# Kernel optimization log

Measured on AMD Instinct MI355X. Metric: run time of the kernel, lower is better.

The kernel has to match this reference:

```python
import jax, jax.numpy as jnp
import numpy as np

N_LAYERS, B, H, D = 24, 16, 32, 64
E = H * D            # 2048
TS_H = 32            # token_shift_hidden_dim
N_BRANCH = 5         # key, receptance, decay, value, bonus
GN_EPS = 1e-3        # keras GroupNormalization default epsilon


def setup_inputs() -> dict:
    key = jax.random.key(0)
    ks = jax.random.split(key, 20)
    s = 0.02
    return {
        "inputs": jax.random.normal(ks[0], (B, E), jnp.float32),
        "state": jax.random.normal(ks[1], (N_LAYERS, 1, B, E), jnp.float32),
        "state_matrix": jax.random.normal(ks[2], (N_LAYERS, B, H, D, D), jnp.float32),
        # stacked branch params, order: key, receptance, decay, value, bonus
        "mus": jax.random.normal(ks[3], (N_BRANCH, E), jnp.float32) * s,
        "lambdas": jax.random.normal(ks[4], (N_BRANCH, E), jnp.float32) * s,
        "Aw": jax.random.normal(ks[5], (N_BRANCH, E, TS_H), jnp.float32) * s,
        "Ab": jnp.zeros((N_BRANCH, TS_H), jnp.float32),
        "Bw": jax.random.normal(ks[6], (N_BRANCH, TS_H, E), jnp.float32) * s,
        "Bb": jnp.zeros((N_BRANCH, E), jnp.float32),
        "MW": jax.random.normal(ks[7], (N_BRANCH, H, D, D), jnp.float32) * s,
        "Mb": jnp.zeros((N_BRANCH, H, D), jnp.float32),
        "gate_mu": jax.random.normal(ks[8], (E,), jnp.float32) * s,
        "gate_W": jax.random.normal(ks[9], (E, E), jnp.float32) * s,
        "gate_b": jnp.zeros((E,), jnp.float32),
        "gn_gamma": jnp.ones((E,), jnp.float32),
        "gn_beta": jnp.zeros((E,), jnp.float32),
        "out_W": jax.random.normal(ks[10], (E, E), jnp.float32) * s,
        "out_b": jnp.zeros((E,), jnp.float32),
        "layer_id": 12,
    }


def reference(inputs, state, state_matrix, mus, lambdas, Aw, Ab, Bw, Bb, MW, Mb,
              gate_mu, gate_W, gate_b, gn_gamma, gn_beta, out_W, out_b, layer_id):
    x = inputs                       # [B, E]
    last_x = state[layer_id, 0]      # [B, E]
    diff = x - last_x

    # ddlerp token shift for all 5 branches at once:
    # lora(x + diff*mu) = lambda + tanh(. @ A) @ B ; out = x + lora * diff
    lora_in = x[None] + diff[None] * mus[:, None]                      # [5, B, E]
    hdn = jnp.tanh(jnp.einsum('sbe,seh->sbh', lora_in, Aw) + Ab[:, None])
    lora = jnp.einsum('sbh,she->sbe', hdn, Bw) + Bb[:, None] + lambdas[:, None]
    ts = (lora * diff[None] + x[None]).reshape(N_BRANCH, B, H, D)      # [5, B, H, D]

    # per-head dense for each branch
    proj = jnp.einsum('sbhd,shde->sbhe', ts, MW) + Mb[:, None]         # [5, B, H, D]
    k, r, w_raw, v, u = proj[0], proj[1], proj[2], proj[3], proj[4]

    g = (x * gate_mu + last_x * (1.0 - gate_mu)) @ gate_W + gate_b     # [B, E]

    kv = k[..., :, None] * v[..., None, :]                             # [B, H, D, D]
    w = jnp.exp(-jnp.exp(w_raw))[..., None]                            # [B, H, D, 1]
    S = state_matrix[layer_id]                                         # [B, H, D, D]
    wkv = kv * u[..., None] + S
    new_S = w * S + kv
    rwkv = jnp.einsum('bhij,bhj->bhi', wkv, r)                         # [B, H, D]

    # group norm: num_heads groups over channel axis
    mean = rwkv.mean(-1, keepdims=True)
    var = rwkv.var(-1, keepdims=True)
    normed = ((rwkv - mean) / jnp.sqrt(var + GN_EPS)).reshape(B, E)
    normed = normed * gn_gamma + gn_beta

    time_mixed = (normed * jax.nn.silu(g)) @ out_W + out_b             # [B, E]

    new_state = state.at[layer_id, 0].set(inputs)
    new_state_matrix = state_matrix.at[layer_id].set(new_S)
    return time_mixed, new_state, new_state_matrix
```

## Files before the change

kernel.cpp:

```cpp
#include <hip/hip_runtime.h>
#include <math.h>

#define NL 24
#define BB 16
#define HH 32
#define DD 64
#define EE 2048
#define TSH 32
#define NB 5
#define BE (BB*EE)
#define STATE_N (NL*BB*EE)
#define GN_EPS 1e-3f

#define NCH 11776
#define C1 2400
#define C2 2200
#define C3 2400
#define C4 2200
#define C5 1776
#define C6 800

__device__ __forceinline__ void sm_chunk(int c, int lid, const float4* __restrict__ sm4,
                                         float4* __restrict__ out4, int tid) {
    int l = c >> 9, rr = c & 511;
    int ls = l + (l >= lid);
    const float4* src = sm4 + (long)(ls * 512 + rr) * 1024;
    float4*       dst = out4 + (long)(ls * 512 + rr) * 1024;
    #pragma unroll
    for (int p = 0; p < 4; ++p) dst[p * 256 + tid] = src[p * 256 + tid];
}

__global__ __launch_bounds__(256) void k1_hdn(
    const float* __restrict__ inputs, const float* __restrict__ state,
    const float* __restrict__ mus, const float* __restrict__ Aw,
    const float* __restrict__ Ab, float* __restrict__ hdn,
    const float4* __restrict__ state4, const float4* __restrict__ inputs4,
    float4* __restrict__ out_state4, float* __restrict__ out_tm,
    float* __restrict__ g, const float* __restrict__ out_b,
    const float* __restrict__ gate_b,
    const float4* __restrict__ sm4, float4* __restrict__ out_sm4,
    const int* __restrict__ lid_p)
{
    int blk = blockIdx.x, tid = threadIdx.x;
    int lid = *lid_p;
    if (blk >= 1104) {
        sm_chunk(blk - 1104, lid, sm4, out_sm4, tid);
        return;
    }
    if (blk >= 848) {
        int idx = (blk - 848) * 256 + tid;
        if (idx < BE) out_tm[idx] = out_b[idx & (EE - 1)];
        else g[idx - BE] = gate_b[(idx - BE) & (EE - 1)];
        return;
    }
    if (blk >= 80) {
        int i = (blk - 80) * 256 + tid;
        int lo = lid * (BE / 4);
        float4 v = (i >= lo && i < lo + BE / 4) ? inputs4[i - lo] : state4[i];
        out_state4[i] = v;
        return;
    }
    int s = blk / BB, b = blk % BB;
    __shared__ float li[EE];
    const float* x  = inputs + b * EE;
    const float* lx = state + lid * BE + b * EE;
    const float* mu = mus + s * EE;
    for (int e = tid; e < EE; e += 256) {
        float xv = x[e];
        li[e] = xv + (xv - lx[e]) * mu[e];
    }
    __syncthreads();
    int h = tid & 31, part = tid >> 5;
    const float* A = Aw + s * EE * TSH;
    float acc = 0.f;
    int e0 = part * 256;
    #pragma unroll 8
    for (int e = e0; e < e0 + 256; ++e) acc += li[e] * A[e * TSH + h];
    __shared__ float red[32][9];
    red[h][part] = acc;
    __syncthreads();
    if (tid < 32) {
        float sum = Ab[s * TSH + tid];
        #pragma unroll
        for (int p = 0; p < 8; ++p) sum += red[tid][p];
        hdn[(s * BB + b) * TSH + tid] = tanhf(sum);
    }
}

__global__ __launch_bounds__(256) void k2_ts(
    const float* __restrict__ inputs, const float* __restrict__ state,
    const float* __restrict__ lambdas, const float* __restrict__ Bw,
    const float* __restrict__ Bb, const float* __restrict__ hdn,
    const float* __restrict__ gate_mu, float* __restrict__ ts,
    float* __restrict__ gx,
    const float4* __restrict__ sm4, float4* __restrict__ out_sm4,
    const int* __restrict__ lid_p)
{
    int blk = blockIdx.x, tid = threadIdx.x;
    int lid = *lid_p;
    if (blk >= 640) {
        sm_chunk(C1 + blk - 640, lid, sm4, out_sm4, tid);
        return;
    }
    int idx = blk * 256 + tid;
    int s = idx / BE, r = idx % BE;
    int b = r / EE, e = r % EE;
    const float* hp = hdn + (s * BB + b) * TSH;
    const float* Bp = Bw + s * TSH * EE + e;
    float acc = Bb[s * EE + e] + lambdas[s * EE + e];
    #pragma unroll
    for (int h = 0; h < TSH; ++h) acc += hp[h] * Bp[h * EE];
    float xv = inputs[r];
    float lxv = state[lid * BE + r];
    ts[idx] = acc * (xv - lxv) + xv;
    if (s == 0) {
        float gm = gate_mu[e];
        gx[r] = xv * gm + lxv * (1.f - gm);
    }
}

__global__ __launch_bounds__(256) void k3_proj(
    const float* __restrict__ ts, const float* __restrict__ MW,
    const float* __restrict__ Mb, float* __restrict__ proj,
    const float4* __restrict__ sm4, float4* __restrict__ out_sm4,
    const int* __restrict__ lid_p)
{
    int bi = blockIdx.x, tid = threadIdx.x;
    if (bi >= 640) {
        int lid = *lid_p;
        sm_chunk(C1 + C2 + bi - 640, lid, sm4, out_sm4, tid);
        return;
    }
    int s = bi / (BB * 8);
    int r = bi % (BB * 8);
    int b = r / 8, hg = r % 8;
    int q = tid >> 6, e = tid & 63;
    int h = hg * 4 + q;
    __shared__ float tl[4][DD];
    tl[q][e] = ts[((s * BB + b) * HH + h) * DD + e];
    __syncthreads();
    const float* M = MW + (s * HH + h) * DD * DD;
    float acc = Mb[(s * HH + h) * DD + e];
    #pragma unroll 8
    for (int d = 0; d < DD; ++d) acc += tl[q][d] * M[d * DD + e];
    proj[((s * BB + b) * HH + h) * DD + e] = acc;
}

template <bool SILU>
__device__ __forceinline__ void mm_block(
    int t, const float* __restrict__ Arows, const float* __restrict__ Grows,
    const float* __restrict__ W, float* __restrict__ out, int tid)
{
    int et = t & 7, kc = t >> 3;
    int e = et * 256 + tid;
    int k0 = kc * 64;
    __shared__ float As[BB][64];
    for (int i = tid; i < BB * 64; i += 256) {
        int b = i >> 6, kk = i & 63;
        float av = Arows[b * EE + k0 + kk];
        if constexpr (SILU) {
            float gv = Grows[b * EE + k0 + kk];
            av *= gv / (1.f + expf(-gv));
        }
        As[b][kk] = av;
    }
    __syncthreads();
    float acc[BB];
    #pragma unroll
    for (int b = 0; b < BB; ++b) acc[b] = 0.f;
    #pragma unroll 8
    for (int kk = 0; kk < 64; ++kk) {
        float wv = W[(k0 + kk) * EE + e];
        #pragma unroll
        for (int b = 0; b < BB; ++b) acc[b] += As[b][kk] * wv;
    }
    #pragma unroll
    for (int b = 0; b < BB; ++b) atomicAdd(&out[b * EE + e], acc[b]);
}

__global__ __launch_bounds__(256) void k4_gate(
    const float* __restrict__ gx, const float* __restrict__ gate_W,
    float* __restrict__ g,
    const float4* __restrict__ sm4, float4* __restrict__ out_sm4,
    const int* __restrict__ lid_p)
{
    int blk = blockIdx.x, tid = threadIdx.x;
    if (blk < 256) { mm_block<false>(blk, gx, nullptr, gate_W, g, tid); return; }
    int lid = *lid_p;
    sm_chunk(C1 + C2 + C3 + blk - 256, lid, sm4, out_sm4, tid);
}

__global__ __launch_bounds__(256) void k5_rwkv(
    const float4* __restrict__ sm4, float4* __restrict__ out_sm4,
    const float* __restrict__ proj,
    const float* __restrict__ gn_gamma, const float* __restrict__ gn_beta,
    float* __restrict__ a_out, const int* __restrict__ lid_p)
{
    int blk = blockIdx.x, tid = threadIdx.x;
    int lid = *lid_p;
    if (blk >= 512) {
        sm_chunk(C1 + C2 + C3 + C4 + blk - 512, lid, sm4, out_sm4, tid);
        return;
    }
    int b = blk / HH, h = blk % HH;
    long base4 = (long)(lid * BB * HH + blk) * (DD * DD / 4);
    int j = tid & 63, q = tid >> 6;
    const float* P = proj + (b * HH + h) * DD + j;
    float kv   = P[0 * BE];
    float rv   = P[1 * BE];
    float wraw = P[2 * BE];
    float vv   = P[3 * BE];
    float uv   = P[4 * BE];
    float wv = expf(-expf(wraw));
    float vr = vv * rv;
    #pragma unroll
    for (int o = 32; o; o >>= 1) vr += __shfl_xor(vr, o);
    __shared__ float rw[DD];
    const float* S = (const float*)(sm4 + base4);
    float* NS = (float*)(out_sm4 + base4);
    for (int ii = 0; ii < 16; ii += 4) {
        int i0 = q * 16 + ii;
        float sv[4], kk[4], ww[4], uu[4], pp[4];
        #pragma unroll
        for (int t = 0; t < 4; ++t) {
            sv[t] = S[(i0 + t) * DD + j];
            kk[t] = __shfl(kv, i0 + t);
            ww[t] = __shfl(wv, i0 + t);
            uu[t] = __shfl(uv, i0 + t);
        }
        #pragma unroll
        for (int t = 0; t < 4; ++t) {
            NS[(i0 + t) * DD + j] = ww[t] * sv[t] + kk[t] * vv;
            pp[t] = sv[t] * rv;
        }
        #pragma unroll
        for (int o = 32; o; o >>= 1) {
            #pragma unroll
            for (int t = 0; t < 4; ++t) pp[t] += __shfl_xor(pp[t], o);
        }
        if (j == 0) {
            #pragma unroll
            for (int t = 0; t < 4; ++t) rw[i0 + t] = kk[t] * uu[t] * vr + pp[t];
        }
    }
    __syncthreads();
    if (tid < DD) {
        float xv = rw[tid];
        float m = xv;
        #pragma unroll
        for (int o = 32; o; o >>= 1) m += __shfl_xor(m, o);
        m *= (1.f / 64.f);
        float d = xv - m;
        float var = d * d;
        #pragma unroll
        for (int o = 32; o; o >>= 1) var += __shfl_xor(var, o);
        var *= (1.f / 64.f);
        float normed = d * rsqrtf(var + GN_EPS);
        int e = h * DD + tid;
        a_out[b * EE + e] = normed * gn_gamma[e] + gn_beta[e];
    }
}

__global__ __launch_bounds__(256) void k6_out(
    const float* __restrict__ a, const float* __restrict__ g,
    const float* __restrict__ out_W, float* __restrict__ out_tm,
    const float4* __restrict__ sm4, float4* __restrict__ out_sm4,
    const int* __restrict__ lid_p)
{
    int blk = blockIdx.x, tid = threadIdx.x;
    if (blk < 256) { mm_block<true>(blk, a, g, out_W, out_tm, tid); return; }
    int lid = *lid_p;
    sm_chunk(C1 + C2 + C3 + C4 + C5 + blk - 256, lid, sm4, out_sm4, tid);
}

extern "C" void kernel_launch(void* const* d_in, const int* in_sizes, int n_in,
                              void* d_out, int out_size, void* d_ws, size_t ws_size,
                              hipStream_t stream) {
    const float* inputs   = (const float*)d_in[0];
    const float* state    = (const float*)d_in[1];
    const float* sm       = (const float*)d_in[2];
    const float* mus      = (const float*)d_in[3];
    const float* lambdas  = (const float*)d_in[4];
    const float* Aw       = (const float*)d_in[5];
    const float* Ab       = (const float*)d_in[6];
    const float* Bw       = (const float*)d_in[7];
    const float* Bb       = (const float*)d_in[8];
    const float* MW       = (const float*)d_in[9];
    const float* Mb       = (const float*)d_in[10];
    const float* gate_mu  = (const float*)d_in[11];
    const float* gate_W   = (const float*)d_in[12];
    const float* gate_b   = (const float*)d_in[13];
    const float* gn_gamma = (const float*)d_in[14];
    const float* gn_beta  = (const float*)d_in[15];
    const float* out_W    = (const float*)d_in[16];
    const float* out_b    = (const float*)d_in[17];
    const int*   lid      = (const int*)d_in[18];

    float* out_tm    = (float*)d_out;
    float* out_state = out_tm + BE;
    float* out_sm    = out_state + STATE_N;

    float* ws   = (float*)d_ws;
    float* ts   = ws;
    float* proj = ts + NB * BE;
    float* hdn  = proj + NB * BE;
    float* gx   = hdn + NB * BB * TSH;
    float* g    = gx + BE;
    float* a    = g + BE;

    k1_hdn<<<1104 + C1, 256, 0, stream>>>(inputs, state, mus, Aw, Ab, hdn,
        (const float4*)state, (const float4*)inputs, (float4*)out_state,
        out_tm, g, out_b, gate_b, (const float4*)sm, (float4*)out_sm, lid);
    k2_ts<<<640 + C2, 256, 0, stream>>>(inputs, state, lambdas, Bw, Bb, hdn,
        gate_mu, ts, gx, (const float4*)sm, (float4*)out_sm, lid);
    k3_proj<<<640 + C3, 256, 0, stream>>>(ts, MW, Mb, proj,
        (const float4*)sm, (float4*)out_sm, lid);
    k4_gate<<<256 + C4, 256, 0, stream>>>(gx, gate_W, g,
        (const float4*)sm, (float4*)out_sm, lid);
    k5_rwkv<<<512 + C5, 256, 0, stream>>>((const float4*)sm, (float4*)out_sm,
        proj, gn_gamma, gn_beta, a, lid);
    k6_out<<<256 + C6, 256, 0, stream>>>(a, g, out_W, out_tm,
        (const float4*)sm, (float4*)out_sm, lid);
}
```

Baseline: 442.5 us.

## Merge gate matmul into projection kernel, move gx to k1, use nontemporal copies

Moves the gate input mix (gx) computation into the first kernel and merges the gate matmul blocks into the per-head projection kernel, cutting the launch count from six to five. The state-matrix copy chunk split across kernels is rebalanced to fit the new schedule. The bulk state and state-matrix copies now use nontemporal loads and stores so they bypass the cache and leave room for the compute data. The risk is an uneven chunk split that lengthens some kernels, and nontemporal hints may not help on this hardware.

```diff
diff --git a/kernel.cpp b/kernel.cpp
--- a/kernel.cpp
+++ b/kernel.cpp
@@ -13,51 +13,69 @@
 #define GN_EPS 1e-3f
 
 #define NCH 11776
-#define C1 2400
-#define C2 2200
-#define C3 2400
-#define C4 2200
-#define C5 1776
-#define C6 800
-
-__device__ __forceinline__ void sm_chunk(int c, int lid, const float4* __restrict__ sm4,
-                                         float4* __restrict__ out4, int tid) {
+#define C1 2700
+#define C2 2500
+#define C3 2100
+#define C4 2400
+#define C5 2076
+
+typedef float nt4 __attribute__((ext_vector_type(4)));
+
+__device__ __forceinline__ void sm_chunk(int c, int lid, const nt4* __restrict__ sm4,
+                                         nt4* __restrict__ out4, int tid) {
     int l = c >> 9, rr = c & 511;
     int ls = l + (l >= lid);
-    const float4* src = sm4 + (long)(ls * 512 + rr) * 1024;
-    float4*       dst = out4 + (long)(ls * 512 + rr) * 1024;
-    #pragma unroll
-    for (int p = 0; p < 4; ++p) dst[p * 256 + tid] = src[p * 256 + tid];
+    const nt4* src = sm4 + (long)(ls * 512 + rr) * 1024;
+    nt4*       dst = out4 + (long)(ls * 512 + rr) * 1024;
+    #pragma unroll
+    for (int p = 0; p < 4; ++p) {
+        nt4 v = __builtin_nontemporal_load(&src[p * 256 + tid]);
+        __builtin_nontemporal_store(v, &dst[p * 256 + tid]);
+    }
 }
 
 __global__ __launch_bounds__(256) void k1_hdn(
     const float* __restrict__ inputs, const float* __restrict__ state,
     const float* __restrict__ mus, const float* __restrict__ Aw,
     const float* __restrict__ Ab, float* __restrict__ hdn,
-    const float4* __restrict__ state4, const float4* __restrict__ inputs4,
-    float4* __restrict__ out_state4, float* __restrict__ out_tm,
+    const nt4* __restrict__ state4, const float4* __restrict__ inputs4,
+    nt4* __restrict__ out_state4, float* __restrict__ out_tm,
     float* __restrict__ g, const float* __restrict__ out_b,
-    const float* __restrict__ gate_b,
-    const float4* __restrict__ sm4, float4* __restrict__ out_sm4,
+    const float* __restrict__ gate_b, const float* __restrict__ gate_mu,
+    float* __restrict__ gx,
+    const nt4* __restrict__ sm4, nt4* __restrict__ out_sm4,
     const int* __restrict__ lid_p)
 {
     int blk = blockIdx.x, tid = threadIdx.x;
     int lid = *lid_p;
-    if (blk >= 1104) {
-        sm_chunk(blk - 1104, lid, sm4, out_sm4, tid);
+    if (blk >= 1232) {
+        sm_chunk(blk - 1232, lid, sm4, out_sm4, tid);
         return;
     }
     if (blk >= 848) {
         int idx = (blk - 848) * 256 + tid;
         if (idx < BE) out_tm[idx] = out_b[idx & (EE - 1)];
-        else g[idx - BE] = gate_b[(idx - BE) & (EE - 1)];
+        else if (idx < 2 * BE) g[idx - BE] = gate_b[(idx - BE) & (EE - 1)];
+        else {
+            int r = idx - 2 * BE;
+            float xv = inputs[r];
+            float lxv = state[lid * BE + r];
+            float gm = gate_mu[r & (EE - 1)];
+            gx[r] = xv * gm + lxv * (1.f - gm);
+        }
         return;
     }
     if (blk >= 80) {
         int i = (blk - 80) * 256 + tid;
         int lo = lid * (BE / 4);
-        float4 v = (i >= lo && i < lo + BE / 4) ? inputs4[i - lo] : state4[i];
-        out_state4[i] = v;
+        if (i >= lo && i < lo + BE / 4) {
+            float4 v = inputs4[i - lo];
+            nt4 w = { v.x, v.y, v.z, v.w };
+            __builtin_nontemporal_store(w, &out_state4[i]);
+        } else {
+            nt4 v = __builtin_nontemporal_load(&state4[i]);
+            __builtin_nontemporal_store(v, &out_state4[i]);
+        }
         return;
     }
     int s = blk / BB, b = blk % BB;
@@ -91,9 +109,8 @@
     const float* __restrict__ inputs, const float* __restrict__ state,
     const float* __restrict__ lambdas, const float* __restrict__ Bw,
     const float* __restrict__ Bb, const float* __restrict__ hdn,
-    const float* __restrict__ gate_mu, float* __restrict__ ts,
-    float* __restrict__ gx,
-    const float4* __restrict__ sm4, float4* __restrict__ out_sm4,
+    float* __restrict__ ts,
+    const nt4* __restrict__ sm4, nt4* __restrict__ out_sm4,
     const int* __restrict__ lid_p)
 {
     int blk = blockIdx.x, tid = threadIdx.x;
@@ -113,37 +130,6 @@
     float xv = inputs[r];
     float lxv = state[lid * BE + r];
     ts[idx] = acc * (xv - lxv) + xv;
-    if (s == 0) {
-        float gm = gate_mu[e];
-        gx[r] = xv * gm + lxv * (1.f - gm);
-    }
-}
-
-__global__ __launch_bounds__(256) void k3_proj(
-    const float* __restrict__ ts, const float* __restrict__ MW,
-    const float* __restrict__ Mb, float* __restrict__ proj,
-    const float4* __restrict__ sm4, float4* __restrict__ out_sm4,
-    const int* __restrict__ lid_p)
-{
-    int bi = blockIdx.x, tid = threadIdx.x;
-    if (bi >= 640) {
-        int lid = *lid_p;
-        sm_chunk(C1 + C2 + bi - 640, lid, sm4, out_sm4, tid);
-        return;
-    }
-    int s = bi / (BB * 8);
-    int r = bi % (BB * 8);
-    int b = r / 8, hg = r % 8;
-    int q = tid >> 6, e = tid & 63;
-    int h = hg * 4 + q;
-    __shared__ float tl[4][DD];
-    tl[q][e] = ts[((s * BB + b) * HH + h) * DD + e];
-    __syncthreads();
-    const float* M = MW + (s * HH + h) * DD * DD;
-    float acc = Mb[(s * HH + h) * DD + e];
-    #pragma unroll 8
-    for (int d = 0; d < DD; ++d) acc += tl[q][d] * M[d * DD + e];
-    proj[((s * BB + b) * HH + h) * DD + e] = acc;
 }
 
 template <bool SILU>
@@ -178,19 +164,40 @@
     for (int b = 0; b < BB; ++b) atomicAdd(&out[b * EE + e], acc[b]);
 }
 
-__global__ __launch_bounds__(256) void k4_gate(
+__global__ __launch_bounds__(256) void k3_proj(
+    const float* __restrict__ ts, const float* __restrict__ MW,
+    const float* __restrict__ Mb, float* __restrict__ proj,
     const float* __restrict__ gx, const float* __restrict__ gate_W,
     float* __restrict__ g,
-    const float4* __restrict__ sm4, float4* __restrict__ out_sm4,
+    const nt4* __restrict__ sm4, nt4* __restrict__ out_sm4,
     const int* __restrict__ lid_p)
 {
-    int blk = blockIdx.x, tid = threadIdx.x;
-    if (blk < 256) { mm_block<false>(blk, gx, nullptr, gate_W, g, tid); return; }
-    int lid = *lid_p;
-    sm_chunk(C1 + C2 + C3 + blk - 256, lid, sm4, out_sm4, tid);
-}
-
-__global__ __launch_bounds__(256) void k5_rwkv(
+    int bi = blockIdx.x, tid = threadIdx.x;
+    if (bi >= 896) {
+        int lid = *lid_p;
+        sm_chunk(C1 + C2 + bi - 896, lid, sm4, out_sm4, tid);
+        return;
+    }
+    if (bi >= 640) {
+        mm_block<false>(bi - 640, gx, nullptr, gate_W, g, tid);
+        return;
+    }
+    int s = bi / (BB * 8);
+    int r = bi % (BB * 8);
+    int b = r / 8, hg = r % 8;
+    int q = tid >> 6, e = tid & 63;
+    int h = hg * 4 + q;
+    __shared__ float tl[4][DD];
+    tl[q][e] = ts[((s * BB + b) * HH + h) * DD + e];
+    __syncthreads();
+    const float* M = MW + (s * HH + h) * DD * DD;
+    float acc = Mb[(s * HH + h) * DD + e];
+    #pragma unroll 8
+    for (int d = 0; d < DD; ++d) acc += tl[q][d] * M[d * DD + e];
+    proj[((s * BB + b) * HH + h) * DD + e] = acc;
+}
+
+__global__ __launch_bounds__(256) void k4_rwkv(
     const float4* __restrict__ sm4, float4* __restrict__ out_sm4,
     const float* __restrict__ proj,
     const float* __restrict__ gn_gamma, const float* __restrict__ gn_beta,
@@ -199,7 +206,8 @@
     int blk = blockIdx.x, tid = threadIdx.x;
     int lid = *lid_p;
     if (blk >= 512) {
-        sm_chunk(C1 + C2 + C3 + C4 + blk - 512, lid, sm4, out_sm4, tid);
+        sm_chunk(C1 + C2 + C3 + blk - 512, lid,
+                 (const nt4*)sm4, (nt4*)out_sm4, tid);
         return;
     }
     int b = blk / HH, h = blk % HH;
@@ -261,16 +269,16 @@
     }
 }
 
-__global__ __launch_bounds__(256) void k6_out(
+__global__ __launch_bounds__(256) void k5_out(
     const float* __restrict__ a, const float* __restrict__ g,
     const float* __restrict__ out_W, float* __restrict__ out_tm,
-    const float4* __restrict__ sm4, float4* __restrict__ out_sm4,
+    const nt4* __restrict__ sm4, nt4* __restrict__ out_sm4,
     const int* __restrict__ lid_p)
 {
     int blk = blockIdx.x, tid = threadIdx.x;
     if (blk < 256) { mm_block<true>(blk, a, g, out_W, out_tm, tid); return; }
     int lid = *lid_p;
-    sm_chunk(C1 + C2 + C3 + C4 + C5 + blk - 256, lid, sm4, out_sm4, tid);
+    sm_chunk(C1 + C2 + C3 + C4 + blk - 256, lid, sm4, out_sm4, tid);
 }
 
 extern "C" void kernel_launch(void* const* d_in, const int* in_sizes, int n_in,
@@ -308,17 +316,16 @@
     float* g    = gx + BE;
     float* a    = g + BE;
 
-    k1_hdn<<<1104 + C1, 256, 0, stream>>>(inputs, state, mus, Aw, Ab, hdn,
-        (const float4*)state, (const float4*)inputs, (float4*)out_state,
-        out_tm, g, out_b, gate_b, (const float4*)sm, (float4*)out_sm, lid);
+    k1_hdn<<<1232 + C1, 256, 0, stream>>>(inputs, state, mus, Aw, Ab, hdn,
+        (const nt4*)state, (const float4*)inputs, (nt4*)out_state,
+        out_tm, g, out_b, gate_b, gate_mu, gx,
+        (const nt4*)sm, (nt4*)out_sm, lid);
     k2_ts<<<640 + C2, 256, 0, stream>>>(inputs, state, lambdas, Bw, Bb, hdn,
-        gate_mu, ts, gx, (const float4*)sm, (float4*)out_sm, lid);
-    k3_proj<<<640 + C3, 256, 0, stream>>>(ts, MW, Mb, proj,
-        (const float4*)sm, (float4*)out_sm, lid);
-    k4_gate<<<256 + C4, 256, 0, stream>>>(gx, gate_W, g,
-        (const float4*)sm, (float4*)out_sm, lid);
-    k5_rwkv<<<512 + C5, 256, 0, stream>>>((const float4*)sm, (float4*)out_sm,
+        ts, (const nt4*)sm, (nt4*)out_sm, lid);
+    k3_proj<<<896 + C3, 256, 0, stream>>>(ts, MW, Mb, proj, gx, gate_W, g,
+        (const nt4*)sm, (nt4*)out_sm, lid);
+    k4_rwkv<<<512 + C4, 256, 0, stream>>>((const float4*)sm, (float4*)out_sm,
         proj, gn_gamma, gn_beta, a, lid);
-    k6_out<<<256 + C6, 256, 0, stream>>>(a, g, out_W, out_tm,
-        (const float4*)sm, (float4*)out_sm, lid);
-}
+    k5_out<<<256 + C5, 256, 0, stream>>>(a, g, out_W, out_tm,
+        (const nt4*)sm, (nt4*)out_sm, lid);
+}
```

After: 436.9 us. About the same (-1.3%).
